# Performance work log

Measured on AMD Instinct MI355X. Metric: run time of the kernel, lower is better.

The kernel has to match this reference:

```python
import jax, jax.numpy as jnp
import numpy as np

E = 512
H = 8
D = E // H  # head_dim = 64
SCALE = D ** -0.5
NEG_INF = float('-inf')


def layer_norm(x, g, b, eps=1e-5):
    mu = jnp.mean(x, axis=-1, keepdims=True)
    var = jnp.var(x, axis=-1, keepdims=True)
    return (x - mu) * jax.lax.rsqrt(var + eps) * g + b


def setup_inputs() -> dict:
    key = jax.random.key(0)
    ks = jax.random.split(key, 16)
    B, Q, K = 4, 2048, 2048
    inp = {
        'query': jax.random.normal(ks[0], (B, Q, E), jnp.float32),
        'key_value': jax.random.normal(ks[1], (B, K, E), jnp.float32),
        'kv_mask': jax.random.randint(ks[2], (B, K), 0, 2) > 0,
        'sparse_mask': jax.random.randint(ks[3], (B, Q, K), 0, 2) > 0,
        'ln_q_g': jnp.ones((E,), jnp.float32),
        'ln_q_b': jnp.zeros((E,), jnp.float32),
        'ln_kv_g': jnp.ones((E,), jnp.float32),
        'ln_kv_b': jnp.zeros((E,), jnp.float32),
        # Linear weights stored as (in, out): y = x @ W + b
        'Wq': jax.random.normal(ks[4], (E, E), jnp.float32) * (E ** -0.5),
        'bq': jnp.zeros((E,), jnp.float32),
        'Wk': jax.random.normal(ks[5], (E, E), jnp.float32) * (E ** -0.5),
        'bk': jnp.zeros((E,), jnp.float32),
        'Wv': jax.random.normal(ks[6], (E, E), jnp.float32) * (E ** -0.5),
        'bv': jnp.zeros((E,), jnp.float32),
        'Wo': jax.random.normal(ks[7], (E, E), jnp.float32) * (E ** -0.5),
        'bo': jnp.zeros((E,), jnp.float32),
    }
    return inp


def reference(query, key_value, kv_mask, sparse_mask,
              ln_q_g, ln_q_b, ln_kv_g, ln_kv_b,
              Wq, bq, Wk, bk, Wv, bv, Wo, bo):
    B, Qn, _ = query.shape
    Kn = key_value.shape[1]
    qn = layer_norm(query, ln_q_g, ln_q_b)
    kvn = layer_norm(key_value, ln_kv_g, ln_kv_b)
    q = (qn @ Wq + bq).reshape(B, Qn, H, D)
    k = (kvn @ Wk + bk).reshape(B, Kn, H, D)
    v = (kvn @ Wv + bv).reshape(B, Kn, H, D)
    # scores: [B, H, Q, K]
    scores = jnp.einsum('bqhd,bkhd->bhqk', q, k) * SCALE
    mask = kv_mask[:, None, None, :] & sparse_mask[:, None, :, :]
    scores = jnp.where(mask, scores, NEG_INF)
    attn = jax.nn.softmax(scores, axis=-1)
    # nan_to_num(0): rows with no valid key -> all-zero weights
    valid_row = jnp.any(mask, axis=-1, keepdims=True)
    attn = jnp.where(valid_row, attn, 0.0)
    out = jnp.einsum('bhqk,bkhd->bqhd', attn, v).reshape(B, Qn, E)
    return out @ Wo + bo
```

## Files before the change

kernel.cpp:

```cpp
#include <hip/hip_runtime.h>
#include <hip/hip_bf16.h>
#include <math.h>

typedef unsigned short ushort_t;
typedef __attribute__((ext_vector_type(8))) __bf16 bf16x8;
typedef __attribute__((ext_vector_type(4))) float f32x4;
typedef __attribute__((ext_vector_type(16))) float f32x16;
typedef __attribute__((ext_vector_type(4))) unsigned int u32x4;

#define E_DIM 512
#define HEADS 8
#define HD 64
#define SEQ 2048
#define NROWS 8192
#define QSCALE 0.18033688011112042f

static __device__ __forceinline__ unsigned short f2b(float f) {
  unsigned int x;
  __builtin_memcpy(&x, &f, 4);
  x += 0x7fffu + ((x >> 16) & 1u);
  return (unsigned short)(x >> 16);
}

static __device__ __forceinline__ unsigned cvt_pk_bf16(float lo, float hi) {
  unsigned r;
  asm("v_cvt_pk_bf16_f32 %0, %1, %2" : "=v"(r) : "v"(lo), "v"(hi));
  return r;
}

static __device__ __forceinline__ float fexp2(float x) {
  float r;
  asm("v_exp_f32 %0, %1" : "=v"(r) : "v"(x));
  return r;
}

static __device__ __forceinline__ unsigned bitmask1(unsigned v, int off) {
#if __has_builtin(__builtin_amdgcn_sbfe)
  return (unsigned)__builtin_amdgcn_sbfe((int)v, off, 1);
#else
  return (unsigned)((int)(v << (31 - off)) >> 31);
#endif
}

static __device__ __forceinline__ int swz(int row, int col) {
  return row * 64 + ((((col >> 3) ^ (row & 7)) & 7) << 3) + (col & 7);
}

static __device__ __forceinline__ void gl2lds16(const ushort_t* g, ushort_t* s) {
#if __has_builtin(__builtin_amdgcn_global_load_lds)
  __builtin_amdgcn_global_load_lds(
      (const __attribute__((address_space(1))) unsigned int*)(uintptr_t)g,
      (__attribute__((address_space(3))) unsigned int*)(uintptr_t)s,
      16, 0, 0);
#else
  int l = threadIdx.x & 63;
  *(u32x4*)(s + l * 8) = *(const u32x4*)g;
#endif
}

__launch_bounds__(256)
__global__ void prep_kernel(const float* __restrict__ Wq, const float* __restrict__ Wk,
                            const float* __restrict__ Wv, const float* __restrict__ Wo,
                            ushort_t* __restrict__ WT,
                            const int* __restrict__ kvm, const int* __restrict__ sp,
                            unsigned long long* __restrict__ bits,
                            const float* __restrict__ xq, const float* __restrict__ xkv,
                            const float* __restrict__ gq, const float* __restrict__ bq,
                            const float* __restrict__ gkv, const float* __restrict__ bkv,
                            ushort_t* __restrict__ yq, ushort_t* __restrict__ ykv) {
  int blk = blockIdx.x;
  int t = threadIdx.x;
  if (blk < 1024) {
    int z = blk >> 8, rem = blk & 255;
    const float* in = (z == 0) ? Wq : (z == 1) ? Wk : (z == 2) ? Wv : Wo;
    ushort_t* o = WT + (size_t)z * E_DIM * E_DIM;
    __shared__ float tile[32 * 33];
    int tx = t & 31, ty = t >> 5;
    int n0 = (rem & 15) * 32, k0 = (rem >> 4) * 32;
#pragma unroll
    for (int i = 0; i < 4; ++i) {
      int k = ty + i * 8;
      tile[k * 33 + tx] = in[(k0 + k) * E_DIM + n0 + tx];
    }
    __syncthreads();
#pragma unroll
    for (int i = 0; i < 4; ++i) {
      int n = ty + i * 8;
      o[(n0 + n) * E_DIM + k0 + tx] = f2b(tile[tx * 33 + n]);
    }
  } else if (blk < 3072) {
    int w = t >> 6, l = t & 63;
    int row = (blk - 1024) * 4 + w;
    int b = row >> 11;
    const int4* sprow = (const int4*)(sp + ((size_t)row << 11));
    const int4* kvrow = (const int4*)(kvm + ((size_t)b << 11));
    unsigned long long* out = bits + ((size_t)row << 5);
#pragma unroll
    for (int it = 0; it < 8; ++it) {
      int4 s4 = sprow[it * 64 + l];
      int4 k4 = kvrow[it * 64 + l];
      unsigned nib = (unsigned)((s4.x && k4.x) ? 1 : 0) | ((s4.y && k4.y) ? 2u : 0)
                   | ((s4.z && k4.z) ? 4u : 0) | ((s4.w && k4.w) ? 8u : 0);
      unsigned long long b0 = __ballot((nib & 1u) != 0);
      unsigned long long b1 = __ballot((nib & 2u) != 0);
      unsigned long long b2 = __ballot((nib & 4u) != 0);
      unsigned long long b3 = __ballot((nib & 8u) != 0);
      if (l < 4) {
        int m16 = l * 16;
        unsigned long long wv = ((b0 >> m16) & 0xFFFFull)
                              | (((b1 >> m16) & 0xFFFFull) << 16)
                              | (((b2 >> m16) & 0xFFFFull) << 32)
                              | (((b3 >> m16) & 0xFFFFull) << 48);
        out[it * 4 + l] = wv;
      }
    }
  } else {
    int idx = blk - 3072;
    int which = idx >> 11;
    const float* x = which ? xkv : xq;
    const float* g = which ? gkv : gq;
    const float* bb = which ? bkv : bq;
    ushort_t* y = which ? ykv : yq;
    int w = t >> 6, l = t & 63;
    int row = (idx & 2047) * 4 + w;
    f32x4 x0 = *(const f32x4*)&x[row * E_DIM + l * 8];
    f32x4 x1 = *(const f32x4*)&x[row * E_DIM + l * 8 + 4];
    float xf[8], s = 0.f, ss = 0.f;
#pragma unroll
    for (int j = 0; j < 8; ++j) {
      xf[j] = (j < 4) ? x0[j] : x1[j - 4];
      s += xf[j];
      ss += xf[j] * xf[j];
    }
#pragma unroll
    for (int off = 32; off > 0; off >>= 1) {
      s += __shfl_xor(s, off);
      ss += __shfl_xor(ss, off);
    }
    float mu = s * (1.f / 512.f);
    float var = fmaxf(ss * (1.f / 512.f) - mu * mu, 0.f);
    float rs = rsqrtf(var + 1e-5f);
    f32x4 g0 = *(const f32x4*)&g[l * 8];
    f32x4 g1 = *(const f32x4*)&g[l * 8 + 4];
    f32x4 b0 = *(const f32x4*)&bb[l * 8];
    f32x4 b1 = *(const f32x4*)&bb[l * 8 + 4];
#pragma unroll
    for (int j = 0; j < 8; ++j) {
      float gv = (j < 4) ? g0[j] : g1[j - 4];
      float bv = (j < 4) ? b0[j] : b1[j - 4];
      y[row * E_DIM + l * 8 + j] = f2b((xf[j] - mu) * rs * gv + bv);
    }
  }
}

template <int MODE>
static __device__ __forceinline__ void gemm_core64(ushort_t* lA, ushort_t* lB,
                                                   const ushort_t* __restrict__ A,
                                                   const ushort_t* __restrict__ WT,
                                                   const float* __restrict__ bias,
                                                   void* Cv, float scale, int m0, int n0) {
  int t = threadIdx.x, w = t >> 6, l = t & 63;
  int quad = l >> 4, l15 = l & 15;
  int wm_ = w >> 1, wn_ = w & 1;
  int csrc = ((l & 7) ^ (l >> 3)) * 8;
  int rln = l >> 3;

  f32x4 acc[4][2] = {};
  for (int kk = 0; kk < E_DIM; kk += 64) {
    __syncthreads();
#pragma unroll
    for (int i = 0; i < 4; ++i) {
      int r0 = i * 32 + w * 8;
      gl2lds16(&A[(size_t)(m0 + r0 + rln) * E_DIM + kk + csrc], &lA[r0 * 64]);
    }
#pragma unroll
    for (int i = 0; i < 2; ++i) {
      int r0 = i * 32 + w * 8;
      gl2lds16(&WT[(size_t)(n0 + r0 + rln) * E_DIM + kk + csrc], &lB[r0 * 64]);
    }
    __syncthreads();
#pragma unroll
    for (int ks = 0; ks < 2; ++ks) {
      bf16x8 af[4], bf[2];
#pragma unroll
      for (int mt = 0; mt < 4; ++mt)
        af[mt] = *(const bf16x8*)&lA[swz(wm_ * 64 + mt * 16 + l15, ks * 32 + quad * 8)];
#pragma unroll
      for (int nt = 0; nt < 2; ++nt)
        bf[nt] = *(const bf16x8*)&lB[swz(wn_ * 32 + nt * 16 + l15, ks * 32 + quad * 8)];
#pragma unroll
      for (int mt = 0; mt < 4; ++mt)
#pragma unroll
        for (int nt = 0; nt < 2; ++nt)
          acc[mt][nt] = __builtin_amdgcn_mfma_f32_16x16x32_bf16(af[mt], bf[nt], acc[mt][nt], 0, 0, 0);
    }
  }

#pragma unroll
  for (int nt = 0; nt < 2; ++nt) {
    int col = n0 + wn_ * 32 + nt * 16 + l15;
    float bv = bias[col];
    if constexpr (MODE == 2) {
      int h = col >> 6, d = col & 63;
#pragma unroll
      for (int mt = 0; mt < 4; ++mt) {
        int row = m0 + wm_ * 64 + mt * 16 + quad * 4;
        int b = row >> 11, k = row & 2047;
        union { ushort_t u[4]; uint2 v; } pk;
#pragma unroll
        for (int r = 0; r < 4; ++r) pk.u[r] = f2b(acc[mt][nt][r] + bv);
        *(uint2*)&((ushort_t*)Cv)[((((size_t)(b * HEADS + h)) * HD + d) << 11) + k] = pk.v;
      }
    } else {
#pragma unroll
      for (int mt = 0; mt < 4; ++mt) {
#pragma unroll
        for (int r = 0; r < 4; ++r) {
          int rowm = m0 + wm_ * 64 + mt * 16 + quad * 4 + r;
          float val = (acc[mt][nt][r] + bv) * scale;
          if constexpr (MODE == 0)
            ((ushort_t*)Cv)[rowm * E_DIM + col] = f2b(val);
          else
            ((float*)Cv)[rowm * E_DIM + col] = val;
        }
      }
    }
  }
}

__launch_bounds__(256)
__global__ void proj3_kernel(const ushort_t* __restrict__ qn, const ushort_t* __restrict__ WTq,
                             const float* __restrict__ bq, ushort_t* __restrict__ qp,
                             const ushort_t* __restrict__ kvn, const ushort_t* __restrict__ WTv,
                             const float* __restrict__ bv, ushort_t* __restrict__ Vt,
                             const ushort_t* __restrict__ WTk, const float* __restrict__ bk,
                             ushort_t* __restrict__ kp, int zbase) {
  __shared__ ushort_t lA[128 * 64];
  __shared__ ushort_t lB[64 * 64];
  int flat = blockIdx.x;
  int chunk = gridDim.x >> 3;
  int work = (flat & 7) * chunk + (flat >> 3);
  int z = zbase + (work >> 9);
  int r = work & 511;
  int m0 = (r >> 3) * 128, n0 = (r & 7) * 64;
  if (z == 0)      gemm_core64<0>(lA, lB, qn,  WTq, bq, qp, QSCALE, m0, n0);
  else if (z == 1) gemm_core64<2>(lA, lB, kvn, WTv, bv, Vt, 1.f,    m0, n0);
  else             gemm_core64<0>(lA, lB, kvn, WTk, bk, kp, 1.f,    m0, n0);
}

__launch_bounds__(256)
__global__ void out_kernel(const ushort_t* __restrict__ A, const ushort_t* __restrict__ WT,
                           const float* __restrict__ bias, float* __restrict__ C) {
  __shared__ ushort_t lA[128 * 64];
  __shared__ ushort_t lB[64 * 64];
  int flat = blockIdx.x;
  int work = (flat & 7) * 64 + (flat >> 3);
  int m0 = (work >> 3) * 128, n0 = (work & 7) * 64;
  gemm_core64<1>(lA, lB, A, WT, bias, C, 1.f, m0, n0);
}

__launch_bounds__(512)
__global__ void attn_kernel(const ushort_t* __restrict__ Qp, const ushort_t* __restrict__ Kp,
                            const ushort_t* __restrict__ Vt,
                            const unsigned long long* __restrict__ bits,
                            ushort_t* __restrict__ ctx) {
  __shared__ __align__(16) char smemb[65536];
  int t = threadIdx.x, w = t >> 6, l = t & 63;
  int qw = w & 1, ks = w >> 1;
  ushort_t* sQ = (ushort_t*)smemb;
  ushort_t* sK = (ushort_t*)(smemb + ks * 8192);
  ushort_t* sV = (ushort_t*)(smemb + 32768 + ks * 8192);
  int l31 = l & 31, half = l >> 5;

  int flat = blockIdx.x;
  int work = (flat & 7) * 128 + (flat >> 3);
  int qblk = work & 31;
  int h = (work >> 5) & 7;
  int b = work >> 8;
  int q0 = qblk * 64;
  int bh = b * HEADS + h;
  int myq = qw * 32 + l31;
  int csrc = ((l & 7) ^ (l >> 3)) * 8;
  int rln = l >> 3;

  gl2lds16(&Qp[(size_t)(b * SEQ + q0 + w * 8 + rln) * E_DIM + h * HD + csrc], &sQ[w * 8 * 64]);
  __syncthreads();
  bf16x8 qf[4];
#pragma unroll
  for (int ds = 0; ds < 4; ++ds)
    qf[ds] = *(const bf16x8*)&sQ[swz(myq, ds * 16 + 8 * half)];

  const unsigned long long* mrow = bits + ((size_t)(b * SEQ + q0 + myq) << 5);
  f32x16 o0 = {}, o1 = {}, lacc = {};
  union { unsigned u[4]; bf16x8 v; } onec;
#pragma unroll
  for (int i = 0; i < 4; ++i) onec.u[i] = 0x3f803f80u;

  for (int t8 = 0; t8 < 8; ++t8) {
    int kt = t8 * 4 + ks;
    int k0 = kt * 64;
    unsigned long long wmask = mrow[kt];
    __syncthreads();
#pragma unroll
    for (int it = 0; it < 4; ++it) {
      int r0 = (it * 2 + qw) * 8;
      gl2lds16(&Kp[(size_t)(b * SEQ + k0 + r0 + rln) * E_DIM + h * HD + csrc], &sK[r0 * 64]);
      gl2lds16(&Vt[((size_t)bh * HD + r0 + rln) * SEQ + k0 + csrc], &sV[r0 * 64]);
    }
    __syncthreads();

    f32x16 s0 = {}, s1 = {};
    __builtin_amdgcn_s_setprio(1);
#pragma unroll
    for (int ds = 0; ds < 4; ++ds) {
      bf16x8 kf0 = *(const bf16x8*)&sK[swz(l31, ds * 16 + 8 * half)];
      bf16x8 kf1 = *(const bf16x8*)&sK[swz(32 + l31, ds * 16 + 8 * half)];
      s0 = __builtin_amdgcn_mfma_f32_32x32x16_bf16(kf0, qf[ds], s0, 0, 0, 0);
      s1 = __builtin_amdgcn_mfma_f32_32x32x16_bf16(kf1, qf[ds], s1, 0, 0, 0);
    }
    __builtin_amdgcn_s_setprio(0);

    unsigned mlo = (unsigned)wmask, mhi = (unsigned)(wmask >> 32);
    bf16x8 pf[4];
#pragma unroll
    for (int kt2 = 0; kt2 < 2; ++kt2) {
      const f32x16& sv = kt2 ? s1 : s0;
      unsigned wa[4], wb[4];
#pragma unroll
      for (int g = 0; g < 4; ++g) {
        int bb = 8 * kt2 + 2 * g + half;
        unsigned q0u = __float_as_uint(fexp2(sv[g * 4 + 0])) & bitmask1(mlo, bb);
        unsigned q1u = __float_as_uint(fexp2(sv[g * 4 + 1])) & bitmask1(mlo, bb + 16);
        unsigned q2u = __float_as_uint(fexp2(sv[g * 4 + 2])) & bitmask1(mhi, bb);
        unsigned q3u = __float_as_uint(fexp2(sv[g * 4 + 3])) & bitmask1(mhi, bb + 16);
        wa[g] = cvt_pk_bf16(__uint_as_float(q0u), __uint_as_float(q1u));
        wb[g] = cvt_pk_bf16(__uint_as_float(q2u), __uint_as_float(q3u));
      }
      asm("v_permlane32_swap_b32 %0, %1" : "+v"(wa[0]), "+v"(wa[1]));
      asm("v_permlane32_swap_b32 %0, %1" : "+v"(wb[0]), "+v"(wb[1]));
      asm("v_permlane32_swap_b32 %0, %1" : "+v"(wa[2]), "+v"(wa[3]));
      asm("v_permlane32_swap_b32 %0, %1" : "+v"(wb[2]), "+v"(wb[3]));
      union { unsigned u[4]; bf16x8 v; } f0, f1;
      f0.u[0] = wa[0]; f0.u[1] = wb[0]; f0.u[2] = wa[1]; f0.u[3] = wb[1];
      f1.u[0] = wa[2]; f1.u[1] = wb[2]; f1.u[2] = wa[3]; f1.u[3] = wb[3];
      pf[kt2 * 2 + 0] = f0.v;
      pf[kt2 * 2 + 1] = f1.v;
    }

    __builtin_amdgcn_s_setprio(1);
#pragma unroll
    for (int ksp = 0; ksp < 4; ++ksp) {
      bf16x8 vf0 = *(const bf16x8*)&sV[swz(l31, ksp * 16 + 8 * half)];
      bf16x8 vf1 = *(const bf16x8*)&sV[swz(32 + l31, ksp * 16 + 8 * half)];
      o0 = __builtin_amdgcn_mfma_f32_32x32x16_bf16(vf0, pf[ksp], o0, 0, 0, 0);
      o1 = __builtin_amdgcn_mfma_f32_32x32x16_bf16(vf1, pf[ksp], o1, 0, 0, 0);
      lacc = __builtin_amdgcn_mfma_f32_32x32x16_bf16(onec.v, pf[ksp], lacc, 0, 0, 0);
    }
    __builtin_amdgcn_s_setprio(0);
  }

  float lsum = lacc[0];

  __syncthreads();
  float* mrg = (float*)smemb;
  if (ks != 0) {
    float* e = mrg + (((ks - 1) * 2 + qw) * 64 + l) * 33;
#pragma unroll
    for (int r = 0; r < 16; ++r) e[r] = o0[r];
#pragma unroll
    for (int r = 0; r < 16; ++r) e[16 + r] = o1[r];
    e[32] = lsum;
  }
  __syncthreads();
  if (ks == 0) {
#pragma unroll
    for (int s3 = 0; s3 < 3; ++s3) {
      const float* e = mrg + ((s3 * 2 + qw) * 64 + l) * 33;
#pragma unroll
      for (int r = 0; r < 16; ++r) o0[r] += e[r];
#pragma unroll
      for (int r = 0; r < 16; ++r) o1[r] += e[16 + r];
      lsum += e[32];
    }
    float inv = (lsum > 0.f) ? 1.f / lsum : 0.f;
    size_t base = (size_t)(b * SEQ + q0 + myq) * E_DIM + h * HD;
#pragma unroll
    for (int dt = 0; dt < 2; ++dt) {
      const f32x16& oo = dt ? o1 : o0;
#pragma unroll
      for (int g = 0; g < 4; ++g) {
        union { ushort_t u[4]; uint2 v; } ov;
#pragma unroll
        for (int r = 0; r < 4; ++r) ov.u[r] = f2b(oo[g * 4 + r] * inv);
        *(uint2*)&ctx[base + dt * 32 + g * 8 + 4 * half] = ov.v;
      }
    }
  }
}

extern "C" void kernel_launch(void* const* d_in, const int* in_sizes, int n_in,
                              void* d_out, int out_size, void* d_ws, size_t ws_size,
                              hipStream_t stream) {
  const float* query     = (const float*)d_in[0];
  const float* key_value = (const float*)d_in[1];
  const int*   kv_mask   = (const int*)d_in[2];
  const int*   sp_mask   = (const int*)d_in[3];
  const float* ln_q_g  = (const float*)d_in[4];
  const float* ln_q_b  = (const float*)d_in[5];
  const float* ln_kv_g = (const float*)d_in[6];
  const float* ln_kv_b = (const float*)d_in[7];
  const float* Wq = (const float*)d_in[8];
  const float* bq = (const float*)d_in[9];
  const float* Wk = (const float*)d_in[10];
  const float* bk = (const float*)d_in[11];
  const float* Wv = (const float*)d_in[12];
  const float* bv = (const float*)d_in[13];
  const float* Wo = (const float*)d_in[14];
  const float* bo = (const float*)d_in[15];

  const size_t NB = (size_t)NROWS * E_DIM;
  char* ws = (char*)d_ws;
  ushort_t* bufA = (ushort_t*)ws;
  ushort_t* bufB = bufA + NB;
  ushort_t* WT   = bufB + NB;
  ushort_t* WTq = WT;
  ushort_t* WTk = WTq + E_DIM * E_DIM;
  ushort_t* WTv = WTk + E_DIM * E_DIM;
  ushort_t* WTo = WTv + E_DIM * E_DIM;
  unsigned long long* bits = (unsigned long long*)(WTo + E_DIM * E_DIM);
  ushort_t* bufC = (ushort_t*)(ws + (20u << 20));

  ushort_t* dlo = (ushort_t*)d_out;
  ushort_t* dhi = dlo + NB;

  bool fused = ws_size >= (28u << 20);
  ushort_t* kp = fused ? bufC : dlo;

  prep_kernel<<<7168, 256, 0, stream>>>(Wq, Wk, Wv, Wo, WT, kv_mask, sp_mask, bits,
                                        query, key_value, ln_q_g, ln_q_b, ln_kv_g, ln_kv_b,
                                        dlo, bufA);

  if (fused) {
    proj3_kernel<<<1536, 256, 0, stream>>>(dlo, WTq, bq, dhi,
                                           bufA, WTv, bv, bufB,
                                           WTk, bk, bufC, 0);
  } else {
    proj3_kernel<<<1024, 256, 0, stream>>>(dlo, WTq, bq, dhi,
                                           bufA, WTv, bv, bufB,
                                           WTk, bk, dlo, 0);
    proj3_kernel<<<512, 256, 0, stream>>>(dlo, WTq, bq, dhi,
                                          bufA, WTv, bv, bufB,
                                          WTk, bk, dlo, 2);
  }

  attn_kernel<<<1024, 512, 0, stream>>>(dhi, kp, bufB, bits, bufA);

  out_kernel<<<512, 256, 0, stream>>>(bufA, WTo, bo, (float*)d_out);
}
```

Baseline: 261.0 us.

## Halve attention block to 4 waves, each processing two key tiles per step

The attention kernel goes from 8 waves to 4 per block. Each wave now handles two 64-key tiles per iteration instead of one, so the key range is split across 2 wave groups rather than 4. This cuts the cross-wave merge of partial outputs and gives each wave more independent MFMA work between barriers. In exchange each wave holds more registers, LDS grows to 72KB, and there are fewer waves per block to hide latency.

```diff
diff --git a/kernel.cpp b/kernel.cpp
--- a/kernel.cpp
+++ b/kernel.cpp
@@ -259,17 +259,48 @@
   gemm_core64<1>(lA, lB, A, WT, bias, C, 1.f, m0, n0);
 }
 
-__launch_bounds__(512)
+static __device__ __forceinline__ void softmax_frag(const f32x16& s0, const f32x16& s1,
+                                                    unsigned mlo, unsigned mhi, int half,
+                                                    bf16x8* pf, f32x16* dummy_unused) {
+#pragma unroll
+  for (int kt2 = 0; kt2 < 2; ++kt2) {
+    const f32x16& sv = kt2 ? s1 : s0;
+    unsigned wa[4], wb[4];
+#pragma unroll
+    for (int g = 0; g < 4; ++g) {
+      int bb = 8 * kt2 + 2 * g + half;
+      unsigned q0u = __float_as_uint(fexp2(sv[g * 4 + 0])) & bitmask1(mlo, bb);
+      unsigned q1u = __float_as_uint(fexp2(sv[g * 4 + 1])) & bitmask1(mlo, bb + 16);
+      unsigned q2u = __float_as_uint(fexp2(sv[g * 4 + 2])) & bitmask1(mhi, bb);
+      unsigned q3u = __float_as_uint(fexp2(sv[g * 4 + 3])) & bitmask1(mhi, bb + 16);
+      wa[g] = cvt_pk_bf16(__uint_as_float(q0u), __uint_as_float(q1u));
+      wb[g] = cvt_pk_bf16(__uint_as_float(q2u), __uint_as_float(q3u));
+    }
+    asm("v_permlane32_swap_b32 %0, %1" : "+v"(wa[0]), "+v"(wa[1]));
+    asm("v_permlane32_swap_b32 %0, %1" : "+v"(wb[0]), "+v"(wb[1]));
+    asm("v_permlane32_swap_b32 %0, %1" : "+v"(wa[2]), "+v"(wa[3]));
+    asm("v_permlane32_swap_b32 %0, %1" : "+v"(wb[2]), "+v"(wb[3]));
+    union { unsigned u[4]; bf16x8 v; } f0, f1;
+    f0.u[0] = wa[0]; f0.u[1] = wb[0]; f0.u[2] = wa[1]; f0.u[3] = wb[1];
+    f1.u[0] = wa[2]; f1.u[1] = wb[2]; f1.u[2] = wa[3]; f1.u[3] = wb[3];
+    pf[kt2 * 2 + 0] = f0.v;
+    pf[kt2 * 2 + 1] = f1.v;
+  }
+}
+
+__launch_bounds__(256)
 __global__ void attn_kernel(const ushort_t* __restrict__ Qp, const ushort_t* __restrict__ Kp,
                             const ushort_t* __restrict__ Vt,
                             const unsigned long long* __restrict__ bits,
                             ushort_t* __restrict__ ctx) {
-  __shared__ __align__(16) char smemb[65536];
+  __shared__ __align__(16) char smemb[73728];
+  ushort_t* sQ = (ushort_t*)smemb;
   int t = threadIdx.x, w = t >> 6, l = t & 63;
   int qw = w & 1, ks = w >> 1;
-  ushort_t* sQ = (ushort_t*)smemb;
-  ushort_t* sK = (ushort_t*)(smemb + ks * 8192);
-  ushort_t* sV = (ushort_t*)(smemb + 32768 + ks * 8192);
+  ushort_t* sKA = (ushort_t*)(smemb + 8192 + ks * 16384);
+  ushort_t* sKB = sKA + 4096;
+  ushort_t* sVA = (ushort_t*)(smemb + 40960 + ks * 16384);
+  ushort_t* sVB = sVA + 4096;
   int l31 = l & 31, half = l >> 5;
 
   int flat = blockIdx.x;
@@ -283,7 +314,11 @@
   int csrc = ((l & 7) ^ (l >> 3)) * 8;
   int rln = l >> 3;
 
-  gl2lds16(&Qp[(size_t)(b * SEQ + q0 + w * 8 + rln) * E_DIM + h * HD + csrc], &sQ[w * 8 * 64]);
+#pragma unroll
+  for (int it = 0; it < 2; ++it) {
+    int r0 = w * 16 + it * 8;
+    gl2lds16(&Qp[(size_t)(b * SEQ + q0 + r0 + rln) * E_DIM + h * HD + csrc], &sQ[r0 * 64]);
+  }
   __syncthreads();
   bf16x8 qf[4];
 #pragma unroll
@@ -297,64 +332,52 @@
   for (int i = 0; i < 4; ++i) onec.u[i] = 0x3f803f80u;
 
   for (int t8 = 0; t8 < 8; ++t8) {
-    int kt = t8 * 4 + ks;
-    int k0 = kt * 64;
-    unsigned long long wmask = mrow[kt];
+    int ktA = t8 * 4 + ks * 2;
+    int kA0 = ktA * 64, kB0 = kA0 + 64;
+    unsigned long long mA = mrow[ktA], mB = mrow[ktA + 1];
     __syncthreads();
 #pragma unroll
     for (int it = 0; it < 4; ++it) {
       int r0 = (it * 2 + qw) * 8;
-      gl2lds16(&Kp[(size_t)(b * SEQ + k0 + r0 + rln) * E_DIM + h * HD + csrc], &sK[r0 * 64]);
-      gl2lds16(&Vt[((size_t)bh * HD + r0 + rln) * SEQ + k0 + csrc], &sV[r0 * 64]);
+      gl2lds16(&Kp[(size_t)(b * SEQ + kA0 + r0 + rln) * E_DIM + h * HD + csrc], &sKA[r0 * 64]);
+      gl2lds16(&Kp[(size_t)(b * SEQ + kB0 + r0 + rln) * E_DIM + h * HD + csrc], &sKB[r0 * 64]);
+      gl2lds16(&Vt[((size_t)bh * HD + r0 + rln) * SEQ + kA0 + csrc], &sVA[r0 * 64]);
+      gl2lds16(&Vt[((size_t)bh * HD + r0 + rln) * SEQ + kB0 + csrc], &sVB[r0 * 64]);
     }
     __syncthreads();
 
-    f32x16 s0 = {}, s1 = {};
+    f32x16 sA0 = {}, sA1 = {}, sB0 = {}, sB1 = {};
     __builtin_amdgcn_s_setprio(1);
 #pragma unroll
     for (int ds = 0; ds < 4; ++ds) {
-      bf16x8 kf0 = *(const bf16x8*)&sK[swz(l31, ds * 16 + 8 * half)];
-      bf16x8 kf1 = *(const bf16x8*)&sK[swz(32 + l31, ds * 16 + 8 * half)];
-      s0 = __builtin_amdgcn_mfma_f32_32x32x16_bf16(kf0, qf[ds], s0, 0, 0, 0);
-      s1 = __builtin_amdgcn_mfma_f32_32x32x16_bf16(kf1, qf[ds], s1, 0, 0, 0);
+      bf16x8 kfA0 = *(const bf16x8*)&sKA[swz(l31, ds * 16 + 8 * half)];
+      bf16x8 kfA1 = *(const bf16x8*)&sKA[swz(32 + l31, ds * 16 + 8 * half)];
+      bf16x8 kfB0 = *(const bf16x8*)&sKB[swz(l31, ds * 16 + 8 * half)];
+      bf16x8 kfB1 = *(const bf16x8*)&sKB[swz(32 + l31, ds * 16 + 8 * half)];
+      sA0 = __builtin_amdgcn_mfma_f32_32x32x16_bf16(kfA0, qf[ds], sA0, 0, 0, 0);
+      sA1 = __builtin_amdgcn_mfma_f32_32x32x16_bf16(kfA1, qf[ds], sA1, 0, 0, 0);
+      sB0 = __builtin_amdgcn_mfma_f32_32x32x16_bf16(kfB0, qf[ds], sB0, 0, 0, 0);
+      sB1 = __builtin_amdgcn_mfma_f32_32x32x16_bf16(kfB1, qf[ds], sB1, 0, 0, 0);
     }
     __builtin_amdgcn_s_setprio(0);
 
-    unsigned mlo = (unsigned)wmask, mhi = (unsigned)(wmask >> 32);
-    bf16x8 pf[4];
-#pragma unroll
-    for (int kt2 = 0; kt2 < 2; ++kt2) {
-      const f32x16& sv = kt2 ? s1 : s0;
-      unsigned wa[4], wb[4];
-#pragma unroll
-      for (int g = 0; g < 4; ++g) {
-        int bb = 8 * kt2 + 2 * g + half;
-        unsigned q0u = __float_as_uint(fexp2(sv[g * 4 + 0])) & bitmask1(mlo, bb);
-        unsigned q1u = __float_as_uint(fexp2(sv[g * 4 + 1])) & bitmask1(mlo, bb + 16);
-        unsigned q2u = __float_as_uint(fexp2(sv[g * 4 + 2])) & bitmask1(mhi, bb);
-        unsigned q3u = __float_as_uint(fexp2(sv[g * 4 + 3])) & bitmask1(mhi, bb + 16);
-        wa[g] = cvt_pk_bf16(__uint_as_float(q0u), __uint_as_float(q1u));
-        wb[g] = cvt_pk_bf16(__uint_as_float(q2u), __uint_as_float(q3u));
-      }
-      asm("v_permlane32_swap_b32 %0, %1" : "+v"(wa[0]), "+v"(wa[1]));
-      asm("v_permlane32_swap_b32 %0, %1" : "+v"(wb[0]), "+v"(wb[1]));
-      asm("v_permlane32_swap_b32 %0, %1" : "+v"(wa[2]), "+v"(wa[3]));
-      asm("v_permlane32_swap_b32 %0, %1" : "+v"(wb[2]), "+v"(wb[3]));
-      union { unsigned u[4]; bf16x8 v; } f0, f1;
-      f0.u[0] = wa[0]; f0.u[1] = wb[0]; f0.u[2] = wa[1]; f0.u[3] = wb[1];
-      f1.u[0] = wa[2]; f1.u[1] = wb[2]; f1.u[2] = wa[3]; f1.u[3] = wb[3];
-      pf[kt2 * 2 + 0] = f0.v;
-      pf[kt2 * 2 + 1] = f1.v;
-    }
+    bf16x8 pfA[4], pfB[4];
+    softmax_frag(sA0, sA1, (unsigned)mA, (unsigned)(mA >> 32), half, pfA, nullptr);
+    softmax_frag(sB0, sB1, (unsigned)mB, (unsigned)(mB >> 32), half, pfB, nullptr);
 
     __builtin_amdgcn_s_setprio(1);
 #pragma unroll
     for (int ksp = 0; ksp < 4; ++ksp) {
-      bf16x8 vf0 = *(const bf16x8*)&sV[swz(l31, ksp * 16 + 8 * half)];
-      bf16x8 vf1 = *(const bf16x8*)&sV[swz(32 + l31, ksp * 16 + 8 * half)];
-      o0 = __builtin_amdgcn_mfma_f32_32x32x16_bf16(vf0, pf[ksp], o0, 0, 0, 0);
-      o1 = __builtin_amdgcn_mfma_f32_32x32x16_bf16(vf1, pf[ksp], o1, 0, 0, 0);
-      lacc = __builtin_amdgcn_mfma_f32_32x32x16_bf16(onec.v, pf[ksp], lacc, 0, 0, 0);
+      bf16x8 vfA0 = *(const bf16x8*)&sVA[swz(l31, ksp * 16 + 8 * half)];
+      bf16x8 vfA1 = *(const bf16x8*)&sVA[swz(32 + l31, ksp * 16 + 8 * half)];
+      o0 = __builtin_amdgcn_mfma_f32_32x32x16_bf16(vfA0, pfA[ksp], o0, 0, 0, 0);
+      o1 = __builtin_amdgcn_mfma_f32_32x32x16_bf16(vfA1, pfA[ksp], o1, 0, 0, 0);
+      lacc = __builtin_amdgcn_mfma_f32_32x32x16_bf16(onec.v, pfA[ksp], lacc, 0, 0, 0);
+      bf16x8 vfB0 = *(const bf16x8*)&sVB[swz(l31, ksp * 16 + 8 * half)];
+      bf16x8 vfB1 = *(const bf16x8*)&sVB[swz(32 + l31, ksp * 16 + 8 * half)];
+      o0 = __builtin_amdgcn_mfma_f32_32x32x16_bf16(vfB0, pfB[ksp], o0, 0, 0, 0);
+      o1 = __builtin_amdgcn_mfma_f32_32x32x16_bf16(vfB1, pfB[ksp], o1, 0, 0, 0);
+      lacc = __builtin_amdgcn_mfma_f32_32x32x16_bf16(onec.v, pfB[ksp], lacc, 0, 0, 0);
     }
     __builtin_amdgcn_s_setprio(0);
   }
@@ -362,9 +385,9 @@
   float lsum = lacc[0];
 
   __syncthreads();
-  float* mrg = (float*)smemb;
-  if (ks != 0) {
-    float* e = mrg + (((ks - 1) * 2 + qw) * 64 + l) * 33;
+  float* mrg = (float*)(smemb + 8192);
+  if (ks == 1) {
+    float* e = mrg + (qw * 64 + l) * 33;
 #pragma unroll
     for (int r = 0; r < 16; ++r) e[r] = o0[r];
 #pragma unroll
@@ -373,15 +396,12 @@
   }
   __syncthreads();
   if (ks == 0) {
-#pragma unroll
-    for (int s3 = 0; s3 < 3; ++s3) {
-      const float* e = mrg + ((s3 * 2 + qw) * 64 + l) * 33;
-#pragma unroll
-      for (int r = 0; r < 16; ++r) o0[r] += e[r];
-#pragma unroll
-      for (int r = 0; r < 16; ++r) o1[r] += e[16 + r];
-      lsum += e[32];
-    }
+    const float* e = mrg + (qw * 64 + l) * 33;
+#pragma unroll
+    for (int r = 0; r < 16; ++r) o0[r] += e[r];
+#pragma unroll
+    for (int r = 0; r < 16; ++r) o1[r] += e[16 + r];
+    lsum += e[32];
     float inv = (lsum > 0.f) ? 1.f / lsum : 0.f;
     size_t base = (size_t)(b * SEQ + q0 + myq) * E_DIM + h * HD;
 #pragma unroll
@@ -453,7 +473,7 @@
                                           WTk, bk, dlo, 2);
   }
 
-  attn_kernel<<<1024, 512, 0, stream>>>(dhi, kp, bufB, bits, bufA);
+  attn_kernel<<<1024, 256, 0, stream>>>(dhi, kp, bufB, bits, bufA);
 
   out_kernel<<<512, 256, 0, stream>>>(bufA, WTo, bo, (float*)d_out);
 }
```

Result: faster. 244.5 us (-6.3%).
